# Kernel tuning notes

Hardware: AMD Instinct MI355X
Metric: run time of the kernel (lower is better)

## Reference

```python
import jax, jax.numpy as jnp
import numpy as np


def setup_inputs() -> dict:
    key = jax.random.key(0)
    k1, k2 = jax.random.split(key)
    B, P, N, M = 8, 32, 1024, 1024
    normalized_receptive_fields = jax.random.normal(k1, (B, P, N, 3), dtype=jnp.float32)
    reconstructed_points = jax.random.normal(k2, (B, P, M, 3), dtype=jnp.float32)
    return {
        "normalized_receptive_fields": normalized_receptive_fields,
        "reconstructed_points": reconstructed_points,
    }


def reference(normalized_receptive_fields, reconstructed_points):
    B, P, M, _ = reconstructed_points.shape
    N = normalized_receptive_fields.shape[2]
    # Faithful to torch: permute(0,1,3,2) then reshape(-1, M, 3).
    x = jnp.transpose(reconstructed_points, (0, 1, 3, 2)).reshape(-1, M, 3)  # (BP, M, 3)
    y = normalized_receptive_fields.reshape(-1, N, 3)                        # (BP, N, 3)
    xx = jnp.sum(x * x, axis=-1)                 # (BP, M)
    yy = jnp.sum(y * y, axis=-1)                 # (BP, N)
    xy = jnp.einsum('bmc,bnc->bmn', x, y)        # (BP, M, N)
    dist = xx[:, :, None] + yy[:, None, :] - 2.0 * xy  # (BP, M, N)
    min_x_to_y = jnp.min(dist, axis=2)           # (BP, M)
    min_y_to_x = jnp.min(dist, axis=1)           # (BP, N)
    return jnp.mean(min_x_to_y) + jnp.mean(min_y_to_x)
```

## Files before the change

### kernel.cpp

```cpp
#include <hip/hip_runtime.h>


#define MM 1024
#define NN 1024
#define THREADS 1024
#define NWAVES 16
#define FINF 3.4e38f

typedef float f32x4 __attribute__((ext_vector_type(4)));
typedef __bf16 bf16x8 __attribute__((ext_vector_type(8)));

#define BT_OFF 0
#define PAD_OFF 65536
#define RS_OFF (PAD_OFF + 2048)
#define LDS_BYTES (RS_OFF + 64)

__device__ __forceinline__ unsigned short bf16_rne(float v) {
    unsigned u = __float_as_uint(v);
    u = u + 0x7FFFu + ((u >> 16) & 1u);
    return (unsigned short)(u >> 16);
}
__device__ __forceinline__ float bf16f(unsigned short h) {
    return __uint_as_float(((unsigned)h) << 16);
}
struct S3 { unsigned short h0, h1, h2; };
__device__ __forceinline__ S3 split3(float v) {
    S3 o;
    o.h0 = bf16_rne(v);
    float r = v - bf16f(o.h0);
    o.h1 = bf16_rne(r);
    float r2 = r - bf16f(o.h1);
    o.h2 = bf16_rne(r2);
    return o;
}
__device__ __forceinline__ unsigned pk(unsigned short a, unsigned short b) {
    return (unsigned)a | ((unsigned)b << 16);
}
__device__ __forceinline__ float min3f(float a, float b, float c) {
    return fminf(fminf(a, b), c);
}
template <int CTRL>
__device__ __forceinline__ float dpp_ror_min(float v) {
    int vi = __float_as_int(v);
    int t  = __builtin_amdgcn_update_dpp(vi, vi, CTRL, 0xf, 0xf, true);
    return fminf(v, __int_as_float(t));
}

__global__ __launch_bounds__(THREADS, 4)
void chamfer_main(const float* __restrict__ nrf,
                  const float* __restrict__ rp,
                  float* __restrict__ out,
                  float inv_bpm, float inv_bpn) {
    __shared__ __align__(16) unsigned char smem[LDS_BYTES];
    float* rowsumS = (float*)(smem + RS_OFF);

    const int bp   = blockIdx.x >> 1;
    const int dir  = blockIdx.x & 1;
    const int tid  = threadIdx.x;
    const int lane = tid & 63;
    const int wave = tid >> 6;
    const int l15  = lane & 15;
    const int g    = lane >> 4;
    const unsigned short ONE = 0x3F80;

    const float* yB = nrf + (size_t)bp * NN * 3;
    const float* xB = rp + (size_t)bp * MM * 3;

    {
        const int c = tid;
        float v0, v1, v2;
        if (dir == 0) {
            v0 = yB[c * 3 + 0]; v1 = yB[c * 3 + 1]; v2 = yB[c * 3 + 2];
        } else {
            const int k = 3 * c;
            v0 = xB[((k    ) & (MM - 1)) * 3 + ((k    ) >> 10)];
            v1 = xB[((k + 1) & (MM - 1)) * 3 + ((k + 1) >> 10)];
            v2 = xB[((k + 2) & (MM - 1)) * 3 + ((k + 2) >> 10)];
        }
        float nn = __builtin_fmaf(v0, v0, __builtin_fmaf(v1, v1, v2 * v2));
        S3 b0 = split3(v0), b1 = split3(v1), b2 = split3(v2), q = split3(nn);
        uint4 qd[4];
        qd[0] = make_uint4(pk(b0.h0, b0.h1), pk(b0.h0, b0.h1), pk(b0.h2, b0.h0), pk(b1.h0, b1.h1));
        qd[1] = make_uint4(pk(b1.h0, b1.h1), pk(b1.h2, b1.h0), pk(b2.h0, b2.h1), pk(b2.h0, b2.h1));
        qd[2] = make_uint4(pk(b2.h2, b2.h0), pk(ONE, ONE), pk(ONE, q.h0), pk(q.h1, q.h2));
        qd[3] = make_uint4(pk(b0.h2, b0.h1), pk(b1.h2, b1.h1), pk(b2.h2, b2.h1), 0u);
        unsigned char* colBase = smem + BT_OFF + (c >> 4) * 1024 + (c & 15) * 64;
        const int rot = (c >> 1) & 3;
        #pragma unroll
        for (int qq = 0; qq < 4; ++qq)
            *(uint4*)(colBase + (((qq + rot) & 3) * 16)) = qd[qq];
    }

    bf16x8 af[4];
    #pragma unroll
    for (int s = 0; s < 4; ++s) {
        const int m = wave * 64 + s * 16 + l15;
        float v0, v1, v2;
        if (dir == 0) {
            const int k = 3 * m;
            v0 = xB[((k    ) & (MM - 1)) * 3 + ((k    ) >> 10)];
            v1 = xB[((k + 1) & (MM - 1)) * 3 + ((k + 1) >> 10)];
            v2 = xB[((k + 2) & (MM - 1)) * 3 + ((k + 2) >> 10)];
        } else {
            v0 = yB[m * 3 + 0]; v1 = yB[m * 3 + 1]; v2 = yB[m * 3 + 2];
        }
        float nn = __builtin_fmaf(v0, v0, __builtin_fmaf(v1, v1, v2 * v2));
        S3 a0 = split3(-2.0f * v0), a1 = split3(-2.0f * v1), a2 = split3(-2.0f * v2);
        S3 p = split3(nn);
        uint4 q0 = make_uint4(pk(a0.h0, a0.h0), pk(a0.h1, a0.h1), pk(a0.h0, a0.h2), pk(a1.h0, a1.h0));
        uint4 q1 = make_uint4(pk(a1.h1, a1.h1), pk(a1.h0, a1.h2), pk(a2.h0, a2.h0), pk(a2.h1, a2.h1));
        uint4 q2 = make_uint4(pk(a2.h0, a2.h2), pk(p.h0, p.h1), pk(p.h2, ONE), pk(ONE, ONE));
        uint4 q3 = make_uint4(pk(a0.h1, a0.h2), pk(a1.h1, a1.h2), pk(a2.h1, a2.h2), 0u);
        uint4 sel = (g == 0) ? q0 : (g == 1) ? q1 : (g == 2) ? q2 : q3;
        union { uint4 u; bf16x8 b; } cv; cv.u = sel;
        af[s] = cv.b;
    }
    __syncthreads();

    const unsigned char* BtBase = smem + BT_OFF + (unsigned)(l15 * 64)
                                + (unsigned)((((g + (l15 >> 1)) & 3) * 16));
    const f32x4 Z = {0.0f, 0.0f, 0.0f, 0.0f};

    float rmin[4][4];
    #pragma unroll
    for (int s = 0; s < 4; ++s)
        #pragma unroll
        for (int j = 0; j < 4; ++j) rmin[s][j] = FINF;

    bf16x8 c0 = *(const bf16x8*)(BtBase);
    bf16x8 c1 = *(const bf16x8*)(BtBase + 1024);
    #pragma unroll 2
    for (int t = 0; t < 64; t += 2) {
        bf16x8 n0 = *(const bf16x8*)(BtBase + (t + 2) * 1024);
        bf16x8 n1 = *(const bf16x8*)(BtBase + (t + 3) * 1024);

        #pragma unroll
        for (int s = 0; s < 4; ++s) {
            f32x4 aA = __builtin_amdgcn_mfma_f32_16x16x32_bf16(af[s], c0, Z, 0, 0, 0);
            f32x4 aB = __builtin_amdgcn_mfma_f32_16x16x32_bf16(af[s], c1, Z, 0, 0, 0);
            #pragma unroll
            for (int j = 0; j < 4; ++j)
                rmin[s][j] = min3f(rmin[s][j], aA[j], aB[j]);
        }
        c0 = n0; c1 = n1;
    }

    float rowsum = 0.0f;
    #pragma unroll
    for (int s = 0; s < 4; ++s) {
        #pragma unroll
        for (int j = 0; j < 4; ++j) {
            float v = rmin[s][j];
            v = dpp_ror_min<0x121>(v);
            v = dpp_ror_min<0x122>(v);
            v = dpp_ror_min<0x124>(v);
            v = dpp_ror_min<0x128>(v);
            rowsum += v;
        }
    }
    rowsum += __int_as_float(__builtin_amdgcn_ds_swizzle(__float_as_int(rowsum), 0x401F));
    rowsum += __int_as_float(__builtin_amdgcn_ds_bpermute((lane ^ 32) << 2, __float_as_int(rowsum)));
    if (lane == 0) rowsumS[wave] = rowsum;
    __syncthreads();

    if (tid < 64) {
        float r = (tid < NWAVES) ? rowsumS[tid] : 0.0f;
        #pragma unroll
        for (int off = 8; off > 0; off >>= 1) r += __shfl_xor(r, off, 64);
        if (tid == 0) atomicAdd(out, r * (dir ? inv_bpn : inv_bpm));
    }
}

extern "C" void kernel_launch(void* const* d_in, const int* in_sizes, int n_in,
                              void* d_out, int out_size, void* d_ws, size_t ws_size,
                              hipStream_t stream) {
    const float* nrf = (const float*)d_in[0];
    const float* rp  = (const float*)d_in[1];
    float* out = (float*)d_out;

    const int BP = in_sizes[1] / (MM * 3);
    const float inv_bpm = 1.0f / (float)(BP * MM);
    const float inv_bpn = 1.0f / (float)(BP * NN);

    (void)hipMemsetAsync(out, 0, sizeof(float), stream);
    chamfer_main<<<BP * 2, THREADS, 0, stream>>>(nrf, rp, out, inv_bpm, inv_bpn);
}
```

Baseline: 86.90 us.

## Compute both Chamfer directions from one distance matrix per batch slice

Before, each (batch, patch) slice launched two blocks, one per direction, and each built the full distance matrix. Now one block builds the matrix once. It takes row minima in registers as before, and takes column minima per MFMA tile with lane swizzle/bpermute reductions. Per-wave column minima go into a new 64KB LDS buffer and are reduced across waves at the end. This halves MFMA work and halves the grid, at the cost of extra VALU and LDS traffic for the column reductions and a larger LDS footprint per block.

```diff
diff --git a/kernel.cpp b/kernel.cpp
--- a/kernel.cpp
+++ b/kernel.cpp
@@ -12,8 +12,10 @@
 
 #define BT_OFF 0
 #define PAD_OFF 65536
-#define RS_OFF (PAD_OFF + 2048)
-#define LDS_BYTES (RS_OFF + 64)
+#define CW_OFF (PAD_OFF + 2048)
+#define RS_OFF (CW_OFF + 65536)
+#define CS_OFF (RS_OFF + 64)
+#define LDS_BYTES (CS_OFF + 64)
 
 __device__ __forceinline__ unsigned short bf16_rne(float v) {
     unsigned u = __float_as_uint(v);
@@ -45,6 +47,13 @@
     int t  = __builtin_amdgcn_update_dpp(vi, vi, CTRL, 0xf, 0xf, true);
     return fminf(v, __int_as_float(t));
 }
+__device__ __forceinline__ float tile_cmin(const f32x4* a) {
+    float u0 = fminf(min3f(a[0][0], a[0][1], a[0][2]), a[0][3]);
+    float u1 = fminf(min3f(a[1][0], a[1][1], a[1][2]), a[1][3]);
+    float u2 = fminf(min3f(a[2][0], a[2][1], a[2][2]), a[2][3]);
+    float u3 = fminf(min3f(a[3][0], a[3][1], a[3][2]), a[3][3]);
+    return fminf(fminf(u0, u1), fminf(u2, u3));
+}
 
 __global__ __launch_bounds__(THREADS, 4)
 void chamfer_main(const float* __restrict__ nrf,
@@ -52,10 +61,11 @@
                   float* __restrict__ out,
                   float inv_bpm, float inv_bpn) {
     __shared__ __align__(16) unsigned char smem[LDS_BYTES];
+    float* colW    = (float*)(smem + CW_OFF);
     float* rowsumS = (float*)(smem + RS_OFF);
-
-    const int bp   = blockIdx.x >> 1;
-    const int dir  = blockIdx.x & 1;
+    float* csumS   = (float*)(smem + CS_OFF);
+
+    const int bp   = blockIdx.x;
     const int tid  = threadIdx.x;
     const int lane = tid & 63;
     const int wave = tid >> 6;
@@ -68,15 +78,7 @@
 
     {
         const int c = tid;
-        float v0, v1, v2;
-        if (dir == 0) {
-            v0 = yB[c * 3 + 0]; v1 = yB[c * 3 + 1]; v2 = yB[c * 3 + 2];
-        } else {
-            const int k = 3 * c;
-            v0 = xB[((k    ) & (MM - 1)) * 3 + ((k    ) >> 10)];
-            v1 = xB[((k + 1) & (MM - 1)) * 3 + ((k + 1) >> 10)];
-            v2 = xB[((k + 2) & (MM - 1)) * 3 + ((k + 2) >> 10)];
-        }
+        float v0 = yB[c * 3 + 0], v1 = yB[c * 3 + 1], v2 = yB[c * 3 + 2];
         float nn = __builtin_fmaf(v0, v0, __builtin_fmaf(v1, v1, v2 * v2));
         S3 b0 = split3(v0), b1 = split3(v1), b2 = split3(v2), q = split3(nn);
         uint4 qd[4];
@@ -95,15 +97,10 @@
     #pragma unroll
     for (int s = 0; s < 4; ++s) {
         const int m = wave * 64 + s * 16 + l15;
-        float v0, v1, v2;
-        if (dir == 0) {
-            const int k = 3 * m;
-            v0 = xB[((k    ) & (MM - 1)) * 3 + ((k    ) >> 10)];
-            v1 = xB[((k + 1) & (MM - 1)) * 3 + ((k + 1) >> 10)];
-            v2 = xB[((k + 2) & (MM - 1)) * 3 + ((k + 2) >> 10)];
-        } else {
-            v0 = yB[m * 3 + 0]; v1 = yB[m * 3 + 1]; v2 = yB[m * 3 + 2];
-        }
+        const int k = 3 * m;
+        float v0 = xB[((k    ) & (MM - 1)) * 3 + ((k    ) >> 10)];
+        float v1 = xB[((k + 1) & (MM - 1)) * 3 + ((k + 1) >> 10)];
+        float v2 = xB[((k + 2) & (MM - 1)) * 3 + ((k + 2) >> 10)];
         float nn = __builtin_fmaf(v0, v0, __builtin_fmaf(v1, v1, v2 * v2));
         S3 a0 = split3(-2.0f * v0), a1 = split3(-2.0f * v1), a2 = split3(-2.0f * v2);
         S3 p = split3(nn);
@@ -120,6 +117,8 @@
     const unsigned char* BtBase = smem + BT_OFF + (unsigned)(l15 * 64)
                                 + (unsigned)((((g + (l15 >> 1)) & 3) * 16));
     const f32x4 Z = {0.0f, 0.0f, 0.0f, 0.0f};
+    const int xaddr32 = (lane ^ 32) << 2;
+    float* colWrow = colW + wave * 1024 + l15;
 
     float rmin[4][4];
     #pragma unroll
@@ -134,13 +133,33 @@
         bf16x8 n0 = *(const bf16x8*)(BtBase + (t + 2) * 1024);
         bf16x8 n1 = *(const bf16x8*)(BtBase + (t + 3) * 1024);
 
+        f32x4 aA[4], aB[4];
         #pragma unroll
         for (int s = 0; s < 4; ++s) {
-            f32x4 aA = __builtin_amdgcn_mfma_f32_16x16x32_bf16(af[s], c0, Z, 0, 0, 0);
-            f32x4 aB = __builtin_amdgcn_mfma_f32_16x16x32_bf16(af[s], c1, Z, 0, 0, 0);
+            aA[s] = __builtin_amdgcn_mfma_f32_16x16x32_bf16(af[s], c0, Z, 0, 0, 0);
+            aB[s] = __builtin_amdgcn_mfma_f32_16x16x32_bf16(af[s], c1, Z, 0, 0, 0);
+        }
+        #pragma unroll
+        for (int s = 0; s < 4; ++s)
             #pragma unroll
             for (int j = 0; j < 4; ++j)
-                rmin[s][j] = min3f(rmin[s][j], aA[j], aB[j]);
+                rmin[s][j] = min3f(rmin[s][j], aA[s][j], aB[s][j]);
+
+        {
+            float cm = tile_cmin(aA);
+            int sw = __builtin_amdgcn_ds_swizzle(__float_as_int(cm), 0x401F);
+            cm = fminf(cm, __int_as_float(sw));
+            int pz = __builtin_amdgcn_ds_bpermute(xaddr32, __float_as_int(cm));
+            cm = fminf(cm, __int_as_float(pz));
+            if (g == 0) colWrow[t * 16] = cm;
+        }
+        {
+            float cm = tile_cmin(aB);
+            int sw = __builtin_amdgcn_ds_swizzle(__float_as_int(cm), 0x401F);
+            cm = fminf(cm, __int_as_float(sw));
+            int pz = __builtin_amdgcn_ds_bpermute(xaddr32, __float_as_int(cm));
+            cm = fminf(cm, __int_as_float(pz));
+            if (g == 0) colWrow[(t + 1) * 16] = cm;
         }
         c0 = n0; c1 = n1;
     }
@@ -159,15 +178,27 @@
         }
     }
     rowsum += __int_as_float(__builtin_amdgcn_ds_swizzle(__float_as_int(rowsum), 0x401F));
-    rowsum += __int_as_float(__builtin_amdgcn_ds_bpermute((lane ^ 32) << 2, __float_as_int(rowsum)));
+    rowsum += __int_as_float(__builtin_amdgcn_ds_bpermute(xaddr32, __float_as_int(rowsum)));
     if (lane == 0) rowsumS[wave] = rowsum;
     __syncthreads();
 
-    if (tid < 64) {
-        float r = (tid < NWAVES) ? rowsumS[tid] : 0.0f;
-        #pragma unroll
-        for (int off = 8; off > 0; off >>= 1) r += __shfl_xor(r, off, 64);
-        if (tid == 0) atomicAdd(out, r * (dir ? inv_bpn : inv_bpm));
+    {
+        const int c = tid;
+        float v = colW[c];
+        #pragma unroll
+        for (int w = 1; w < NWAVES; ++w) v = fminf(v, colW[w * 1024 + c]);
+        float csum = v;
+        #pragma unroll
+        for (int off = 32; off > 0; off >>= 1) csum += __shfl_xor(csum, off, 64);
+        if (lane == 0) csumS[wave] = csum;
+    }
+    __syncthreads();
+
+    if (tid == 0) {
+        float rs = 0.0f, cs = 0.0f;
+        #pragma unroll
+        for (int w = 0; w < NWAVES; ++w) { rs += rowsumS[w]; cs += csumS[w]; }
+        atomicAdd(out, rs * inv_bpm + cs * inv_bpn);
     }
 }
 
@@ -183,5 +214,5 @@
     const float inv_bpn = 1.0f / (float)(BP * NN);
 
     (void)hipMemsetAsync(out, 0, sizeof(float), stream);
-    chamfer_main<<<BP * 2, THREADS, 0, stream>>>(nrf, rp, out, inv_bpm, inv_bpn);
-}
+    chamfer_main<<<BP, THREADS, 0, stream>>>(nrf, rp, out, inv_bpm, inv_bpn);
+}
```

After: 86.74 us. About the same (-0.2%).
